# Optimization experiments

Hardware: AMD Instinct MI355X
Metric: run time of the kernel (lower is better)

Reference implementation:

```python
import jax, jax.numpy as jnp
import numpy as np
import math

HIDDEN = 2048
HEADS = 16
HEAD_DIM = HIDDEN // HEADS
RANK = HIDDEN // 2  # rank_ratio=0.5
B, S = 1, 4096


def setup_inputs() -> dict:
    key = jax.random.key(0)
    ks = jax.random.split(key, 10)
    sd = lambda fan_in: 1.0 / math.sqrt(fan_in)
    inp = {
        "hidden_states": jax.random.normal(ks[0], (B, S, HIDDEN), dtype=jnp.float32),
        "attention_mask": jnp.zeros((B, 1, S, S), dtype=jnp.float32),
        # low-rank projection weights; Linear weight shape is [out, in]
        "q_V": jax.random.uniform(ks[1], (RANK, HIDDEN), jnp.float32, -sd(HIDDEN), sd(HIDDEN)),
        "q_U": jax.random.uniform(ks[2], (HIDDEN, RANK), jnp.float32, -sd(RANK), sd(RANK)),
        "k_V": jax.random.uniform(ks[3], (RANK, HIDDEN), jnp.float32, -sd(HIDDEN), sd(HIDDEN)),
        "k_U": jax.random.uniform(ks[4], (HIDDEN, RANK), jnp.float32, -sd(RANK), sd(RANK)),
        "v_V": jax.random.uniform(ks[5], (RANK, HIDDEN), jnp.float32, -sd(HIDDEN), sd(HIDDEN)),
        "v_U": jax.random.uniform(ks[6], (HIDDEN, RANK), jnp.float32, -sd(RANK), sd(RANK)),
        "o_W": jax.random.uniform(ks[7], (HIDDEN, HIDDEN), jnp.float32, -sd(HIDDEN), sd(HIDDEN)),
        "o_b": jax.random.uniform(ks[8], (HIDDEN,), jnp.float32, -sd(HIDDEN), sd(HIDDEN)),
    }
    return inp


def _split_heads(x):
    # [B,S,HIDDEN] -> [B,H,S,Dh]
    b, s, _ = x.shape
    return x.reshape(b, s, HEADS, HEAD_DIM).transpose(0, 2, 1, 3)


def reference(hidden_states, attention_mask, q_V, q_U, k_V, k_U, v_V, v_U, o_W, o_b):
    # low-rank QKV: x @ V^T @ U^T
    q = _split_heads((hidden_states @ q_V.T) @ q_U.T)
    k = _split_heads((hidden_states @ k_V.T) @ k_U.T)
    v = _split_heads((hidden_states @ v_V.T) @ v_U.T)
    scores = jnp.einsum("bhqd,bhkd->bhqk", q, k) / math.sqrt(HEAD_DIM)
    scores = scores + attention_mask
    attn = jax.nn.softmax(scores, axis=-1)
    out = jnp.einsum("bhqk,bhkd->bhqd", attn, v)
    out = out.transpose(0, 2, 1, 3).reshape(hidden_states.shape[0], hidden_states.shape[1], HIDDEN)
    out = out @ o_W.T + o_b
    return out
```

## Files before the change

kernel.cpp:

```cpp
#include <hip/hip_runtime.h>

#define HIDDEN 2048
#define HEADS 16
#define HD 128
#define RANK 1024
#define SEQ 4096

typedef __bf16 bf16_t;
typedef __bf16 bf16x8 __attribute__((ext_vector_type(8)));
typedef __bf16 bf16x4 __attribute__((ext_vector_type(4)));
typedef float f32x4 __attribute__((ext_vector_type(4)));
typedef short s16x4 __attribute__((ext_vector_type(4)));

#define MFMA_BF16(a, b, c) __builtin_amdgcn_mfma_f32_16x16x32_bf16((a), (b), (c), 0, 0, 0)

__device__ __forceinline__ s16x4 bc4(bf16x4 v) {
  union { bf16x4 b; s16x4 s; } u;
  u.b = v;
  return u.s;
}
__device__ __forceinline__ f32x4 mfma16_bf16(bf16x4 a, bf16x4 b, f32x4 c) {
  return __builtin_amdgcn_mfma_f32_16x16x16bf16_1k(bc4(a), bc4(b), c, 0, 0, 0);
}

__device__ __forceinline__ void gload16(const bf16_t* g, bf16_t* l) {
  __builtin_amdgcn_global_load_lds(
      (const __attribute__((address_space(1))) unsigned int*)g,
      (__attribute__((address_space(3))) unsigned int*)l, 16, 0, 0);
}

struct CastSeg { const float* s; bf16_t* d; int n4; };
struct CastArgs { CastSeg seg[8]; };

__global__ __launch_bounds__(256) void cast_bf16_kernel(CastArgs a) {
  const int stride = gridDim.x * blockDim.x;
  const int tid0 = blockIdx.x * blockDim.x + threadIdx.x;
#pragma unroll
  for (int i = 0; i < 8; i++) {
    const float4* src = (const float4*)a.seg[i].s;
    bf16x4* dst = (bf16x4*)a.seg[i].d;
    const int n4 = a.seg[i].n4;
    for (int j = tid0; j < n4; j += stride) {
      float4 v = src[j];
      dst[j] = bf16x4{(bf16_t)v.x, (bf16_t)v.y, (bf16_t)v.z, (bf16_t)v.w};
    }
  }
}

__global__ __launch_bounds__(256) void transpose_kernel(const bf16_t* __restrict__ src,
                                                        bf16_t* __restrict__ dst) {
  __shared__ bf16_t Ls[64][68];
  const int s0 = blockIdx.x * 64, c0 = blockIdx.y * 64;
  const int t = threadIdx.x;
  const int r = t >> 3, c8 = t & 7;
#pragma unroll
  for (int p = 0; p < 2; p++) {
    int row = r + p * 32;
    *reinterpret_cast<bf16x8*>(&Ls[row][c8 * 8]) =
        *reinterpret_cast<const bf16x8*>(src + (size_t)(s0 + row) * HIDDEN + c0 + c8 * 8);
  }
  __syncthreads();
#pragma unroll
  for (int p = 0; p < 2; p++) {
    int crow = r + p * 32;
    bf16x8 v;
#pragma unroll
    for (int j = 0; j < 8; j++) v[j] = Ls[c8 * 8 + j][crow];
    *reinterpret_cast<bf16x8*>(dst + (size_t)(c0 + crow) * SEQ + s0 + c8 * 8) = v;
  }
}

template <bool OUT_F32>
__global__ __launch_bounds__(256) void gemm3(const bf16_t* __restrict__ A, int lda, int aOff,
                                             const bf16_t* __restrict__ W0,
                                             const bf16_t* __restrict__ W1,
                                             const bf16_t* __restrict__ W2,
                                             int nPerThird, int K,
                                             void* __restrict__ Cp, int ldc, size_t cOff,
                                             const float* __restrict__ bias) {
  __shared__ bf16_t As[128 * 32];
  __shared__ bf16_t Bs[128 * 32];
  const int tid = threadIdx.x, lane = tid & 63, wave = tid >> 6;
  const int wr = wave >> 1, wc = wave & 1, quad = lane >> 4, l15 = lane & 15;
  const int n0g = blockIdx.x * 128;
  const int third = n0g / nPerThird;
  const int n0 = n0g - third * nPerThird;
  const bf16_t* W = third == 0 ? W0 : (third == 1 ? W1 : W2);
  const bf16_t* Ab = A + (size_t)third * aOff;
  const int m0 = blockIdx.y * 128;

  f32x4 acc[4][4];
#pragma unroll
  for (int i = 0; i < 4; i++)
#pragma unroll
    for (int j = 0; j < 4; j++) acc[i][j] = f32x4{0.f, 0.f, 0.f, 0.f};

  const int KT = K >> 5;
  for (int kt = 0; kt < KT; ++kt) {
#pragma unroll
    for (int i = 0; i < 2; i++) {
      int slot = (wave * 2 + i) * 64 + lane;
      int row = slot >> 2, cp = slot & 3;
      int cl = cp ^ ((row >> 1) & 3);
      gload16(Ab + (size_t)(m0 + row) * lda + kt * 32 + cl * 8, As + (size_t)(wave * 2 + i) * 512);
    }
#pragma unroll
    for (int i = 0; i < 2; i++) {
      int slot = (wave * 2 + i) * 64 + lane;
      int row = slot >> 2, cp = slot & 3;
      int cl = cp ^ ((row >> 1) & 3);
      gload16(W + (size_t)(n0 + row) * K + kt * 32 + cl * 8, Bs + (size_t)(wave * 2 + i) * 512);
    }
    __syncthreads();

    bf16x8 af[4], bfr[4];
#pragma unroll
    for (int mt = 0; mt < 4; mt++) {
      int row = wr * 64 + mt * 16 + l15;
      int phys = quad ^ ((row >> 1) & 3);
      af[mt] = *reinterpret_cast<const bf16x8*>(As + row * 32 + phys * 8);
    }
#pragma unroll
    for (int nt = 0; nt < 4; nt++) {
      int row = wc * 64 + nt * 16 + l15;
      int phys = quad ^ ((row >> 1) & 3);
      bfr[nt] = *reinterpret_cast<const bf16x8*>(Bs + row * 32 + phys * 8);
    }
#pragma unroll
    for (int mt = 0; mt < 4; mt++)
#pragma unroll
      for (int nt = 0; nt < 4; nt++) acc[mt][nt] = MFMA_BF16(af[mt], bfr[nt], acc[mt][nt]);
    __syncthreads();
  }

#pragma unroll
  for (int nt = 0; nt < 4; nt++) {
    int col = n0 + wc * 64 + nt * 16 + l15;
    float bv = 0.f;
    if constexpr (OUT_F32) bv = bias[col];
#pragma unroll
    for (int mt = 0; mt < 4; mt++) {
      int rowb = m0 + wr * 64 + mt * 16 + quad * 4;
#pragma unroll
      for (int r = 0; r < 4; r++) {
        float vx = acc[mt][nt][r];
        if constexpr (OUT_F32)
          ((float*)Cp + (size_t)third * cOff)[(size_t)(rowb + r) * ldc + col] = vx + bv;
        else
          ((bf16_t*)Cp + (size_t)third * cOff)[(size_t)(rowb + r) * ldc + col] = (bf16_t)vx;
      }
    }
  }
}

__global__ __launch_bounds__(256, 2) void attn_kernel(const bf16_t* __restrict__ qb,
                                                      const bf16_t* __restrict__ kb,
                                                      const bf16_t* __restrict__ vtp,
                                                      const float* __restrict__ mask,
                                                      bf16_t* __restrict__ ao) {
  __shared__ bf16_t Ks[2][64 * 128];
  __shared__ bf16_t Vs[2][128 * 64];
  const int tid = threadIdx.x, lane = tid & 63, w = tid >> 6;
  const int quad = lane >> 4, l15 = lane & 15;
  const int head = blockIdx.x, q0 = blockIdx.y * 128;
  const float kScale = 0.088388347648318447f * 1.4426950408889634f;
  const float LOG2E = 1.4426950408889634f;

  bf16x8 qf[2][4];
#pragma unroll
  for (int qt = 0; qt < 2; qt++)
#pragma unroll
    for (int ks = 0; ks < 4; ks++)
      qf[qt][ks] = *reinterpret_cast<const bf16x8*>(
          qb + (size_t)(q0 + w * 32 + qt * 16 + l15) * HIDDEN + head * HD + ks * 32 + quad * 8);

  f32x4 O[8][2];
#pragma unroll
  for (int dt = 0; dt < 8; dt++)
#pragma unroll
    for (int qt = 0; qt < 2; qt++) O[dt][qt] = f32x4{0.f, 0.f, 0.f, 0.f};
  float lacc[2] = {0.f, 0.f};

  auto stageKV = [&](int kt, int buf) {
    const int sk0 = kt * 64;
#pragma unroll
    for (int i = 0; i < 4; i++) {
      int slot = (w * 4 + i) * 64 + lane;
      int row = slot >> 4, cp = slot & 15;
      int cl = cp ^ (row & 7);
      gload16(kb + (size_t)(sk0 + row) * HIDDEN + head * HD + cl * 8,
              &Ks[buf][(size_t)(w * 4 + i) * 512]);
    }
#pragma unroll
    for (int i = 0; i < 4; i++) {
      int slot = (w * 4 + i) * 64 + lane;
      int row = slot >> 3, cp = slot & 7;
      int cl = cp ^ (row & 7);
      gload16(vtp + (size_t)(head * HD + row) * SEQ + sk0 + cl * 8,
              &Vs[buf][(size_t)(w * 4 + i) * 512]);
    }
  };

  stageKV(0, 0);

  for (int kt = 0; kt < SEQ / 64; ++kt) {
    const int sk0 = kt * 64;
    const int buf = kt & 1;
    __syncthreads();
    stageKV(kt + 1, buf ^ 1);

    f32x4 mv[4][2];
#pragma unroll
    for (int ktile = 0; ktile < 4; ktile++)
#pragma unroll
      for (int qt = 0; qt < 2; qt++)
        mv[ktile][qt] = *reinterpret_cast<const f32x4*>(
            mask + (size_t)(q0 + w * 32 + qt * 16 + l15) * SEQ + sk0 + ktile * 16 + quad * 4);

    f32x4 sacc[4][2];
#pragma unroll
    for (int ktile = 0; ktile < 4; ktile++)
#pragma unroll
      for (int qt = 0; qt < 2; qt++) sacc[ktile][qt] = f32x4{0.f, 0.f, 0.f, 0.f};
#pragma unroll
    for (int ks = 0; ks < 4; ks++) {
#pragma unroll
      for (int ktile = 0; ktile < 4; ktile++) {
        int row = ktile * 16 + l15;
        int phys = (ks * 4 + quad) ^ (row & 7);
        bf16x8 ak = *reinterpret_cast<const bf16x8*>(&Ks[buf][row * 128 + phys * 8]);
#pragma unroll
        for (int qt = 0; qt < 2; qt++) sacc[ktile][qt] = MFMA_BF16(ak, qf[qt][ks], sacc[ktile][qt]);
      }
    }

    bf16x4 pk[4][2];
#pragma unroll
    for (int ktile = 0; ktile < 4; ktile++)
#pragma unroll
      for (int qt = 0; qt < 2; qt++) {
        f32x4 e;
#pragma unroll
        for (int r = 0; r < 4; r++)
          e[r] = exp2f(sacc[ktile][qt][r] * kScale + mv[ktile][qt][r] * LOG2E);
        lacc[qt] += (e[0] + e[1]) + (e[2] + e[3]);
        pk[ktile][qt] = bf16x4{(bf16_t)e[0], (bf16_t)e[1], (bf16_t)e[2], (bf16_t)e[3]};
      }

#pragma unroll
    for (int ks = 0; ks < 4; ks++) {
      int klocal = ks * 16 + quad * 4;
      int chunk = klocal >> 3, within = klocal & 7;
#pragma unroll
      for (int dt = 0; dt < 8; dt++) {
        int row = dt * 16 + l15;
        int phys = chunk ^ (row & 7);
        bf16x4 av = *reinterpret_cast<const bf16x4*>(&Vs[buf][row * 64 + phys * 8 + within]);
#pragma unroll
        for (int qt = 0; qt < 2; qt++) O[dt][qt] = mfma16_bf16(av, pk[ks][qt], O[dt][qt]);
      }
    }
  }

#pragma unroll
  for (int qt = 0; qt < 2; qt++) {
    float l = lacc[qt];
    l += __shfl_xor(l, 16, 64);
    l += __shfl_xor(l, 32, 64);
    lacc[qt] = 1.f / l;
  }
#pragma unroll
  for (int dt = 0; dt < 8; dt++)
#pragma unroll
    for (int qt = 0; qt < 2; qt++) {
      int q = q0 + w * 32 + qt * 16 + l15;
      int d = head * HD + dt * 16 + quad * 4;
      f32x4 o = O[dt][qt];
      bf16x4 ov = {(bf16_t)(o[0] * lacc[qt]), (bf16_t)(o[1] * lacc[qt]),
                   (bf16_t)(o[2] * lacc[qt]), (bf16_t)(o[3] * lacc[qt])};
      *reinterpret_cast<bf16x4*>(ao + (size_t)q * HIDDEN + d) = ov;
    }
}

extern "C" void kernel_launch(void* const* d_in, const int* in_sizes, int n_in,
                              void* d_out, int out_size, void* d_ws, size_t ws_size,
                              hipStream_t stream) {
  (void)in_sizes; (void)n_in; (void)out_size; (void)ws_size;
  const float* x = (const float*)d_in[0];
  const float* mask = (const float*)d_in[1];
  const float* qV = (const float*)d_in[2];
  const float* qU = (const float*)d_in[3];
  const float* kV = (const float*)d_in[4];
  const float* kU = (const float*)d_in[5];
  const float* vV = (const float*)d_in[6];
  const float* vU = (const float*)d_in[7];
  const float* oW = (const float*)d_in[8];
  const float* ob = (const float*)d_in[9];
  float* out = (float*)d_out;

  char* ws = (char*)d_ws;
  const size_t MB = 1ull << 20;
  bf16_t* xb  = (bf16_t*)(ws);
  bf16_t* tmp = (bf16_t*)(ws + 16 * MB);
  bf16_t* qkv = (bf16_t*)(ws + 40 * MB);
  bf16_t* qVb = (bf16_t*)(ws + 88 * MB);
  bf16_t* qUb = (bf16_t*)(ws + 92 * MB);
  bf16_t* kVb = (bf16_t*)(ws + 96 * MB);
  bf16_t* kUb = (bf16_t*)(ws + 100 * MB);
  bf16_t* vVb = (bf16_t*)(ws + 104 * MB);
  bf16_t* vUb = (bf16_t*)(ws + 108 * MB);
  bf16_t* oWb = (bf16_t*)(ws + 112 * MB);

  CastArgs ca;
  ca.seg[0] = {x, xb, SEQ * HIDDEN / 4};
  ca.seg[1] = {qV, qVb, RANK * HIDDEN / 4};
  ca.seg[2] = {qU, qUb, HIDDEN * RANK / 4};
  ca.seg[3] = {kV, kVb, RANK * HIDDEN / 4};
  ca.seg[4] = {kU, kUb, HIDDEN * RANK / 4};
  ca.seg[5] = {vV, vVb, RANK * HIDDEN / 4};
  ca.seg[6] = {vU, vUb, HIDDEN * RANK / 4};
  ca.seg[7] = {oW, oWb, HIDDEN * HIDDEN / 4};
  cast_bf16_kernel<<<2048, 256, 0, stream>>>(ca);

  gemm3<false><<<dim3(24, 32), 256, 0, stream>>>(xb, HIDDEN, 0, qVb, kVb, vVb, RANK, HIDDEN,
                                                 tmp, 3 * RANK, (size_t)RANK, nullptr);
  gemm3<false><<<dim3(48, 32), 256, 0, stream>>>(tmp, 3 * RANK, RANK, qUb, kUb, vUb, HIDDEN, RANK,
                                                 qkv, HIDDEN, (size_t)SEQ * HIDDEN, nullptr);
  transpose_kernel<<<dim3(SEQ / 64, HIDDEN / 64), 256, 0, stream>>>(qkv + 2 * (size_t)SEQ * HIDDEN, tmp);
  attn_kernel<<<dim3(HEADS, SEQ / 128), 256, 0, stream>>>(qkv, qkv + (size_t)SEQ * HIDDEN, tmp, mask, xb);
  gemm3<true><<<dim3(16, 32), 256, 0, stream>>>(xb, HIDDEN, 0, oWb, oWb, oWb, HIDDEN, HIDDEN,
                                                out, HIDDEN, 0, ob);
}
```

Baseline: 612.2 us.

## Use 16x16x32 MFMA for PV via key-row permutation and fold softmax scale into Q

```diff
diff --git a/kernel.cpp b/kernel.cpp
--- a/kernel.cpp
+++ b/kernel.cpp
@@ -10,18 +10,8 @@
 typedef __bf16 bf16x8 __attribute__((ext_vector_type(8)));
 typedef __bf16 bf16x4 __attribute__((ext_vector_type(4)));
 typedef float f32x4 __attribute__((ext_vector_type(4)));
-typedef short s16x4 __attribute__((ext_vector_type(4)));
 
 #define MFMA_BF16(a, b, c) __builtin_amdgcn_mfma_f32_16x16x32_bf16((a), (b), (c), 0, 0, 0)
-
-__device__ __forceinline__ s16x4 bc4(bf16x4 v) {
-  union { bf16x4 b; s16x4 s; } u;
-  u.b = v;
-  return u.s;
-}
-__device__ __forceinline__ f32x4 mfma16_bf16(bf16x4 a, bf16x4 b, f32x4 c) {
-  return __builtin_amdgcn_mfma_f32_16x16x16bf16_1k(bc4(a), bc4(b), c, 0, 0, 0);
-}
 
 __device__ __forceinline__ void gload16(const bf16_t* g, bf16_t* l) {
   __builtin_amdgcn_global_load_lds(
@@ -77,7 +67,7 @@
                                              const bf16_t* __restrict__ W2,
                                              int nPerThird, int K,
                                              void* __restrict__ Cp, int ldc, size_t cOff,
-                                             const float* __restrict__ bias) {
+                                             const float* __restrict__ bias, float s0) {
   __shared__ bf16_t As[128 * 32];
   __shared__ bf16_t Bs[128 * 32];
   const int tid = threadIdx.x, lane = tid & 63, wave = tid >> 6;
@@ -88,6 +78,7 @@
   const bf16_t* W = third == 0 ? W0 : (third == 1 ? W1 : W2);
   const bf16_t* Ab = A + (size_t)third * aOff;
   const int m0 = blockIdx.y * 128;
+  const float sc = (third == 0) ? s0 : 1.f;
 
   f32x4 acc[4][4];
 #pragma unroll
@@ -147,7 +138,7 @@
         if constexpr (OUT_F32)
           ((float*)Cp + (size_t)third * cOff)[(size_t)(rowb + r) * ldc + col] = vx + bv;
         else
-          ((bf16_t*)Cp + (size_t)third * cOff)[(size_t)(rowb + r) * ldc + col] = (bf16_t)vx;
+          ((bf16_t*)Cp + (size_t)third * cOff)[(size_t)(rowb + r) * ldc + col] = (bf16_t)(vx * sc);
       }
     }
   }
@@ -163,7 +154,6 @@
   const int tid = threadIdx.x, lane = tid & 63, w = tid >> 6;
   const int quad = lane >> 4, l15 = lane & 15;
   const int head = blockIdx.x, q0 = blockIdx.y * 128;
-  const float kScale = 0.088388347648318447f * 1.4426950408889634f;
   const float LOG2E = 1.4426950408889634f;
 
   bf16x8 qf[2][4];
@@ -187,7 +177,7 @@
     for (int i = 0; i < 4; i++) {
       int slot = (w * 4 + i) * 64 + lane;
       int row = slot >> 4, cp = slot & 15;
-      int cl = cp ^ (row & 7);
+      int cl = cp ^ ((row & 3) | ((row & 8) >> 1));
       gload16(kb + (size_t)(sk0 + row) * HIDDEN + head * HD + cl * 8,
               &Ks[buf][(size_t)(w * 4 + i) * 512]);
     }
@@ -203,63 +193,74 @@
 
   stageKV(0, 0);
 
+  const int sK = (l15 & 3) | (((l15 >> 2) & 1) << 2);
+  const int rA0 = ((l15 >> 2) << 3) + (l15 & 3);
+
   for (int kt = 0; kt < SEQ / 64; ++kt) {
     const int sk0 = kt * 64;
     const int buf = kt & 1;
     __syncthreads();
     stageKV(kt + 1, buf ^ 1);
 
-    f32x4 mv[4][2];
-#pragma unroll
-    for (int ktile = 0; ktile < 4; ktile++)
-#pragma unroll
-      for (int qt = 0; qt < 2; qt++)
-        mv[ktile][qt] = *reinterpret_cast<const f32x4*>(
-            mask + (size_t)(q0 + w * 32 + qt * 16 + l15) * SEQ + sk0 + ktile * 16 + quad * 4);
-
-    f32x4 sacc[4][2];
-#pragma unroll
-    for (int ktile = 0; ktile < 4; ktile++)
-#pragma unroll
-      for (int qt = 0; qt < 2; qt++) sacc[ktile][qt] = f32x4{0.f, 0.f, 0.f, 0.f};
+    f32x4 mv[2][2][2];
+#pragma unroll
+    for (int kp = 0; kp < 2; kp++)
+#pragma unroll
+      for (int sub = 0; sub < 2; sub++)
+#pragma unroll
+        for (int qt = 0; qt < 2; qt++)
+          mv[kp][sub][qt] = *reinterpret_cast<const f32x4*>(
+              mask + (size_t)(q0 + w * 32 + qt * 16 + l15) * SEQ + sk0 + kp * 32 + quad * 8 +
+              sub * 4);
+
+    f32x4 sacc[2][2][2];
+#pragma unroll
+    for (int kp = 0; kp < 2; kp++)
+#pragma unroll
+      for (int sub = 0; sub < 2; sub++)
+#pragma unroll
+        for (int qt = 0; qt < 2; qt++) sacc[kp][sub][qt] = f32x4{0.f, 0.f, 0.f, 0.f};
 #pragma unroll
     for (int ks = 0; ks < 4; ks++) {
-#pragma unroll
-      for (int ktile = 0; ktile < 4; ktile++) {
-        int row = ktile * 16 + l15;
-        int phys = (ks * 4 + quad) ^ (row & 7);
-        bf16x8 ak = *reinterpret_cast<const bf16x8*>(&Ks[buf][row * 128 + phys * 8]);
-#pragma unroll
-        for (int qt = 0; qt < 2; qt++) sacc[ktile][qt] = MFMA_BF16(ak, qf[qt][ks], sacc[ktile][qt]);
-      }
-    }
-
-    bf16x4 pk[4][2];
-#pragma unroll
-    for (int ktile = 0; ktile < 4; ktile++)
-#pragma unroll
-      for (int qt = 0; qt < 2; qt++) {
-        f32x4 e;
-#pragma unroll
-        for (int r = 0; r < 4; r++)
-          e[r] = exp2f(sacc[ktile][qt][r] * kScale + mv[ktile][qt][r] * LOG2E);
-        lacc[qt] += (e[0] + e[1]) + (e[2] + e[3]);
-        pk[ktile][qt] = bf16x4{(bf16_t)e[0], (bf16_t)e[1], (bf16_t)e[2], (bf16_t)e[3]};
-      }
-
-#pragma unroll
-    for (int ks = 0; ks < 4; ks++) {
-      int klocal = ks * 16 + quad * 4;
-      int chunk = klocal >> 3, within = klocal & 7;
+      int phys = (ks * 4 + quad) ^ sK;
+#pragma unroll
+      for (int kp = 0; kp < 2; kp++)
+#pragma unroll
+        for (int sub = 0; sub < 2; sub++) {
+          int rowA = kp * 32 + sub * 4 + rA0;
+          bf16x8 ak = *reinterpret_cast<const bf16x8*>(&Ks[buf][rowA * 128 + phys * 8]);
+#pragma unroll
+          for (int qt = 0; qt < 2; qt++)
+            sacc[kp][sub][qt] = MFMA_BF16(ak, qf[qt][ks], sacc[kp][sub][qt]);
+        }
+    }
+
+    bf16x8 pf[2][2];
+#pragma unroll
+    for (int kp = 0; kp < 2; kp++)
+#pragma unroll
+      for (int sub = 0; sub < 2; sub++)
+#pragma unroll
+        for (int qt = 0; qt < 2; qt++) {
+          f32x4 e;
+#pragma unroll
+          for (int r = 0; r < 4; r++)
+            e[r] = exp2f(sacc[kp][sub][qt][r] + mv[kp][sub][qt][r] * LOG2E);
+          lacc[qt] += (e[0] + e[1]) + (e[2] + e[3]);
+#pragma unroll
+          for (int r = 0; r < 4; r++) pf[kp][qt][sub * 4 + r] = (bf16_t)e[r];
+        }
+
+#pragma unroll
+    for (int kp = 0; kp < 2; kp++)
 #pragma unroll
       for (int dt = 0; dt < 8; dt++) {
         int row = dt * 16 + l15;
-        int phys = chunk ^ (row & 7);
-        bf16x4 av = *reinterpret_cast<const bf16x4*>(&Vs[buf][row * 64 + phys * 8 + within]);
-#pragma unroll
-        for (int qt = 0; qt < 2; qt++) O[dt][qt] = mfma16_bf16(av, pk[ks][qt], O[dt][qt]);
+        int phys = (kp * 4 + quad) ^ (l15 & 7);
+        bf16x8 av = *reinterpret_cast<const bf16x8*>(&Vs[buf][row * 64 + phys * 8]);
+#pragma unroll
+        for (int qt = 0; qt < 2; qt++) O[dt][qt] = MFMA_BF16(av, pf[kp][qt], O[dt][qt]);
       }
-    }
   }
 
 #pragma unroll
@@ -311,6 +312,8 @@
   bf16_t* vUb = (bf16_t*)(ws + 108 * MB);
   bf16_t* oWb = (bf16_t*)(ws + 112 * MB);
 
+  const float kQScale = 0.088388347648318447f * 1.4426950408889634f;
+
   CastArgs ca;
   ca.seg[0] = {x, xb, SEQ * HIDDEN / 4};
   ca.seg[1] = {qV, qVb, RANK * HIDDEN / 4};
@@ -323,11 +326,12 @@
   cast_bf16_kernel<<<2048, 256, 0, stream>>>(ca);
 
   gemm3<false><<<dim3(24, 32), 256, 0, stream>>>(xb, HIDDEN, 0, qVb, kVb, vVb, RANK, HIDDEN,
-                                                 tmp, 3 * RANK, (size_t)RANK, nullptr);
+                                                 tmp, 3 * RANK, (size_t)RANK, nullptr, 1.f);
   gemm3<false><<<dim3(48, 32), 256, 0, stream>>>(tmp, 3 * RANK, RANK, qUb, kUb, vUb, HIDDEN, RANK,
-                                                 qkv, HIDDEN, (size_t)SEQ * HIDDEN, nullptr);
+                                                 qkv, HIDDEN, (size_t)SEQ * HIDDEN, nullptr,
+                                                 kQScale);
   transpose_kernel<<<dim3(SEQ / 64, HIDDEN / 64), 256, 0, stream>>>(qkv + 2 * (size_t)SEQ * HIDDEN, tmp);
   attn_kernel<<<dim3(HEADS, SEQ / 128), 256, 0, stream>>>(qkv, qkv + (size_t)SEQ * HIDDEN, tmp, mask, xb);
   gemm3<true><<<dim3(16, 32), 256, 0, stream>>>(xb, HIDDEN, 0, oWb, oWb, oWb, HIDDEN, HIDDEN,
-                                                out, HIDDEN, 0, ob);
-}
+                                                out, HIDDEN, 0, ob, 1.f);
+}
```

Result: faster. 596.1 us (-2.6%).
